# Performance work log

Measured on AMD Instinct MI355X. Metric: run time of the kernel, lower is better.

The kernel has to match this reference:

```python
import jax, jax.numpy as jnp
import numpy as np

LATENT, H, A, L, BOS = 256, 512, 64, 128, 0


def setup_inputs() -> dict:
    key = jax.random.key(0)
    ks = jax.random.split(key, 20)
    s = 0.05
    return {
        "latent": jax.random.normal(ks[0], (4096, LATENT), jnp.float32),
        "target": jax.random.normal(ks[1], (4096, L, A), jnp.float32),
        # latent dense decoder: Linear(LATENT,H), Tanh, Linear(H,H), Tanh, Linear(H,H)
        "Wd1": jax.random.normal(ks[2], (H, LATENT), jnp.float32) * s,
        "bd1": jnp.zeros((H,), jnp.float32),
        "Wd2": jax.random.normal(ks[3], (H, H), jnp.float32) * s,
        "bd2": jnp.zeros((H,), jnp.float32),
        "Wd3": jax.random.normal(ks[4], (H, H), jnp.float32) * s,
        "bd3": jnp.zeros((H,), jnp.float32),
        # GRU (torch layout: W_ih [3H,A], W_hh [3H,H], gate order r,z,n)
        "W_ih": jax.random.normal(ks[5], (3 * H, A), jnp.float32) * s,
        "W_hh": jax.random.normal(ks[6], (3 * H, H), jnp.float32) * s,
        "b_ih": jnp.zeros((3 * H,), jnp.float32),
        "b_hh": jnp.zeros((3 * H,), jnp.float32),
        # per-step dense decoder: Linear(H,H), Tanh, Linear(H,A), Tanh, Linear(A,A)
        "Wm1": jax.random.normal(ks[7], (H, H), jnp.float32) * s,
        "bm1": jnp.zeros((H,), jnp.float32),
        "Wm2": jax.random.normal(ks[8], (A, H), jnp.float32) * s,
        "bm2": jnp.zeros((A,), jnp.float32),
        "Wm3": jax.random.normal(ks[9], (A, A), jnp.float32) * s,
        "bm3": jnp.zeros((A,), jnp.float32),
    }


def reference(latent, target, Wd1, bd1, Wd2, bd2, Wd3, bd3,
              W_ih, W_hh, b_ih, b_hh, Wm1, bm1, Wm2, bm2, Wm3, bm3):
    B = latent.shape[0]
    # initial hidden from latent: Linear-Tanh-Linear-Tanh-Linear
    h = jnp.tanh(latent @ Wd1.T + bd1)
    h = jnp.tanh(h @ Wd2.T + bd2)
    h = h @ Wd3.T + bd3  # [B, H]

    # BOS pseudo one-hot: -16 everywhere, +16 at BOS index
    bos = jnp.full((B, A), -16.0, jnp.float32).at[:, BOS].set(16.0)

    # teacher forcing: step i (1..L-1) consumes [bos, target[:,1], ..., target[:,L-2]]
    xs = jnp.concatenate([bos[None], jnp.swapaxes(target[:, 1:L - 1], 0, 1)], axis=0)  # [L-1, B, A]

    def step(h, x):
        gi = x @ W_ih.T + b_ih  # [B, 3H]
        gh = h @ W_hh.T + b_hh
        ir, iz, inn = jnp.split(gi, 3, axis=-1)
        hr, hz, hn = jnp.split(gh, 3, axis=-1)
        r = jax.nn.sigmoid(ir + hr)
        z = jax.nn.sigmoid(iz + hz)
        n = jnp.tanh(inn + r * hn)
        h_new = (1.0 - z) * n + z * h
        p = jnp.tanh(h_new @ Wm1.T + bm1)
        p = jnp.tanh(p @ Wm2.T + bm2)
        pred = p @ Wm3.T + bm3  # [B, A]
        return h_new, pred

    _, preds = jax.lax.scan(step, h, xs)  # preds: [L-1, B, A]
    y = jnp.concatenate([bos[None], preds], axis=0)  # [L, B, A]
    return jnp.swapaxes(y, 0, 1)  # [B, L, A]
```

## Files before the change

### kernel.cpp

```cpp
#include <hip/hip_runtime.h>
#include <math.h>
#include <stdint.h>

#define BATCH 4096
#define LATENT 256
#define H 512
#define A 64
#define SEQL 128
#define KCAT 576
#define NSTEP 127
#define SEGLEN 16
#define NSEG 8

#define MB 256
#define JB 32
#define BST 584
#define AS_ELEMS (3 * 256 * 32)
#define BS_ELEMS (96 * BST)
#define GRU_LDS ((AS_ELEMS + BS_ELEMS) * 2)

typedef __bf16 bf16x8 __attribute__((ext_vector_type(8)));
typedef float f32x4 __attribute__((ext_vector_type(4)));
typedef uint16_t u16x8 __attribute__((ext_vector_type(8)));

__device__ __forceinline__ uint16_t f2bf(float f) {
    union { float f; uint32_t u; } v; v.f = f;
    uint32_t u = v.u + 0x7FFFu + ((v.u >> 16) & 1u);
    return (uint16_t)(u >> 16);
}

__device__ __forceinline__ float fast_sig(float x) {
    return __fdividef(1.0f, 1.0f + __expf(-x));
}
__device__ __forceinline__ float fast_tanh(float x) {
    return __fdividef(2.0f, 1.0f + __expf(-2.0f * x)) - 1.0f;
}

__device__ __forceinline__ f32x4 mfma16(bf16x8 a, bf16x8 b, f32x4 c) {
    return __builtin_amdgcn_mfma_f32_16x16x32_bf16(a, b, c, 0, 0, 0);
}

__device__ __forceinline__ void load_lds16(const void* g, void* l) {
    __builtin_amdgcn_global_load_lds(
        (const __attribute__((address_space(1))) uint32_t*)g,
        (__attribute__((address_space(3))) uint32_t*)l, 16, 0, 0);
}


__global__ __launch_bounds__(256) void cvt_bf16_kernel(const float* __restrict__ src,
                                                       uint16_t* __restrict__ dst, int n) {
    int idx = (blockIdx.x * 256 + threadIdx.x) * 4;
    if (idx < n) {
        float4 v = *(const float4*)(src + idx);
        dst[idx + 0] = f2bf(v.x); dst[idx + 1] = f2bf(v.y);
        dst[idx + 2] = f2bf(v.z); dst[idx + 3] = f2bf(v.w);
    }
}

__global__ __launch_bounds__(256) void wcat_kernel(const float* __restrict__ W_ih,
                                                   const float* __restrict__ W_hh,
                                                   uint16_t* __restrict__ Wcat) {
    int idx = blockIdx.x * 256 + threadIdx.x;
    if (idx < 1536 * KCAT) {
        int row = idx / KCAT, col = idx - row * KCAT;
        float v = (col < 64) ? W_ih[row * 64 + col] : W_hh[row * 512 + col - 64];
        Wcat[idx] = f2bf(v);
    }
}

__global__ __launch_bounds__(256) void bias_kernel(const float* __restrict__ b_ih,
                                                   const float* __restrict__ b_hh,
                                                   float* __restrict__ biases) {
    int idx = blockIdx.x * 256 + threadIdx.x;
    if (idx < 2048) {
        int seg = idx >> 9, j = idx & 511;
        float v;
        if (seg == 0) v = b_ih[j] + b_hh[j];
        else if (seg == 1) v = b_ih[512 + j] + b_hh[512 + j];
        else if (seg == 2) v = b_ih[1024 + j];
        else v = b_hh[1024 + j];
        biases[idx] = v;
    }
}

__global__ __launch_bounds__(256) void xseg_kernel(const float* __restrict__ target,
                                                   uint16_t* __restrict__ X,
                                                   int t0, int ns) {
    int idx = blockIdx.x * 256 + threadIdx.x;
    int e = idx * 4;
    int a = e & 63;
    int b = (e >> 6) & (BATCH - 1);
    int sl = e >> 18;
    int t = t0 + sl;
    ushort4 o;
    if (t == 0) {
        o.x = f2bf((a == 0) ? 16.0f : -16.0f);
        uint16_t m16 = f2bf(-16.0f);
        o.y = m16; o.z = m16; o.w = m16;
    } else {
        float4 v = *(const float4*)(target + ((size_t)b * SEQL + t) * A + a);
        o.x = f2bf(v.x); o.y = f2bf(v.y); o.z = f2bf(v.z); o.w = f2bf(v.w);
    }
    *(ushort4*)(X + e) = o;
}

__global__ __launch_bounds__(256) void bosout_kernel(float* __restrict__ out) {
    int idx = blockIdx.x * 256 + threadIdx.x;
    int a = idx & (A - 1);
    int b = idx >> 6;
    out[(size_t)b * SEQL * A + a] = (a == 0) ? 16.0f : -16.0f;
}

__global__ __launch_bounds__(256)
void gemm_kernel(const uint16_t* __restrict__ Abf, int lda,
                 const uint16_t* __restrict__ Wbf,
                 const float* __restrict__ bias,
                 uint16_t* __restrict__ outb, float* __restrict__ outf,
                 int ldc, int K, int do_tanh)
{
    __shared__ __align__(16) uint16_t As[128 * 32];
    __shared__ __align__(16) uint16_t Bs[128 * 32];

    const int tid = threadIdx.x;
    const int w = tid >> 6, l = tid & 63;
    const int quad = l >> 4, lan = l & 15;
    const int m0 = blockIdx.y * 128;
    const int n0 = blockIdx.x * 128;
    const int wm = (w >> 1) * 64;
    const int wn = (w & 1) * 64;

    f32x4 acc[4][4];
#pragma unroll
    for (int i = 0; i < 4; ++i)
#pragma unroll
        for (int j = 0; j < 4; ++j) acc[i][j] = (f32x4){0.f, 0.f, 0.f, 0.f};

    const int arow = (l >> 2);
    const int kc8 = (l & 3) * 8;

    for (int k0 = 0; k0 < K; k0 += 32) {
        __syncthreads();
#pragma unroll
        for (int i = 0; i < 2; ++i) {
            int row = i * 64 + w * 16 + arow;
            load_lds16(Abf + (size_t)(m0 + row) * lda + k0 + kc8,
                       As + i * 2048 + w * 512 + l * 8);
        }
#pragma unroll
        for (int i = 0; i < 2; ++i) {
            int row = i * 64 + w * 16 + arow;
            load_lds16(Wbf + (size_t)(n0 + row) * K + k0 + kc8,
                       Bs + i * 2048 + w * 512 + l * 8);
        }
        __syncthreads();

        bf16x8 af[4], bf[4];
#pragma unroll
        for (int mi = 0; mi < 4; ++mi)
            af[mi] = *(const bf16x8*)(As + (wm + mi * 16 + lan) * 32 + quad * 8);
#pragma unroll
        for (int nj = 0; nj < 4; ++nj)
            bf[nj] = *(const bf16x8*)(Bs + (wn + nj * 16 + lan) * 32 + quad * 8);
#pragma unroll
        for (int mi = 0; mi < 4; ++mi)
#pragma unroll
            for (int nj = 0; nj < 4; ++nj)
                acc[mi][nj] = mfma16(af[mi], bf[nj], acc[mi][nj]);
    }

#pragma unroll
    for (int mi = 0; mi < 4; ++mi) {
#pragma unroll
        for (int nj = 0; nj < 4; ++nj) {
#pragma unroll
            for (int reg = 0; reg < 4; ++reg) {
                int m = m0 + wm + mi * 16 + quad * 4 + reg;
                int n = n0 + wn + nj * 16 + lan;
                float v = acc[mi][nj][reg] + bias[n];
                if (do_tanh) v = fast_tanh(v);
                if (outf) outf[(size_t)m * ldc + n] = v;
                if (outb) outb[(size_t)m * ldc + n] = f2bf(v);
            }
        }
    }
}

__global__ __launch_bounds__(512)
void gru_seg_kernel(const uint16_t* __restrict__ Xseg,
                    const uint16_t* __restrict__ Wcat,
                    const float* __restrict__ biases,
                    const uint16_t* __restrict__ hprev0,
                    float* __restrict__ hA,
                    uint16_t* __restrict__ hall,
                    uint32_t* __restrict__ cnt,
                    int nsteps)
{
    extern __shared__ __align__(16) uint16_t lds[];
    uint16_t* As = lds;
    uint16_t* Bs = lds + AS_ELEMS;

    const int tid = threadIdx.x;
    const int bid = blockIdx.x;
    const int xcd = bid & 7;
    const int kk  = bid >> 3;
    const int jb  = kk & 15;
    const int mg  = xcd + ((kk >> 4) << 3);
    const int j0  = jb * JB;
    const int mbase = mg * MB;

    const int w = tid >> 6, l = tid & 63;
    const int quad = l >> 4, lan = l & 15;
    const int wm = (w >> 1) * 64;
    const int wj = (w & 1) * 16;
    const int jcol = j0 + wj + lan;

    float hreg[4][4];
#pragma unroll
    for (int mi = 0; mi < 4; ++mi)
#pragma unroll
        for (int r = 0; r < 4; ++r)
            hreg[mi][r] = hA[(size_t)(mbase + wm + mi * 16 + quad * 4 + r) * H + jcol];
    const float br = biases[jcol], bz = biases[512 + jcol];
    const float bi = biases[1024 + jcol], bh = biases[1536 + jcol];
    __builtin_amdgcn_sched_barrier(0);
    asm volatile("s_waitcnt vmcnt(0)");
    __builtin_amdgcn_sched_barrier(0);

    for (int i = tid; i < 96 * 72; i += 512) {
        int row = i / 72, c = i - row * 72;
        int wrow = ((row >> 5) << 9) + j0 + (row & 31);
        uint4 v = *(const uint4*)(Wcat + (size_t)wrow * KCAT + c * 8);
        *(uint4*)(Bs + row * BST + c * 8) = v;
    }
    __builtin_amdgcn_sched_barrier(0);

    auto stage = [&](int s2, int kt2, int bsel) {
        const uint16_t* P; int ld;
        if (kt2 < 2) { P = Xseg + ((size_t)s2 * BATCH + mbase) * 64 + kt2 * 32; ld = 64; }
        else {
            const uint16_t* hs = (s2 == 0) ? hprev0 : hall + (size_t)(s2 - 1) * (BATCH * H);
            P = hs + (size_t)mbase * H + (kt2 - 2) * 32; ld = 512;
        }
#pragma unroll
        for (int i = 0; i < 2; ++i) {
            int g = i * 512 + tid;
            int row = g & 255, c = g >> 8;
            load_lds16(P + (size_t)row * ld + c * 8, As + bsel * 8192 + g * 8);
        }
    };

    stage(0, 0, 0);
    stage(0, 1, 1);
    __builtin_amdgcn_sched_barrier(0);
    asm volatile("s_waitcnt lgkmcnt(0)");
    __builtin_amdgcn_s_barrier();
    __builtin_amdgcn_sched_barrier(0);

    f32x4 acc[4][4];
#pragma unroll
    for (int i = 0; i < 4; ++i)
#pragma unroll
        for (int j = 0; j < 4; ++j) acc[i][j] = (f32x4){0.f, 0.f, 0.f, 0.f};

    const int N = 18 * nsteps;
    int bufc = 0;

    for (int s = 0; s < nsteps; ++s) {
        for (int kt = 0; kt < 18; ++kt) {
            const int ts = s * 18 + kt;
            if (kt == 0 && s > 0) {
                if (tid == 0) {
                    const uint32_t* fl = cnt + mg * SEGLEN + (s - 1);
                    while (__hip_atomic_load(fl, __ATOMIC_RELAXED,
                                             __HIP_MEMORY_SCOPE_AGENT) < 16u)
                        __builtin_amdgcn_s_sleep(8);
                }
                __builtin_amdgcn_s_barrier();
                __builtin_amdgcn_sched_barrier(0);
            }
            if (ts + 2 < N) {
                int kt2 = kt + 2, s2 = s;
                if (kt2 >= 18) { kt2 -= 18; ++s2; }
                int sb = bufc + 2; if (sb >= 3) sb -= 3;
                stage(s2, kt2, sb);
            }
            __builtin_amdgcn_sched_barrier(0);
            if (ts + 2 < N)      asm volatile("s_waitcnt vmcnt(4)");
            else if (ts + 1 < N) asm volatile("s_waitcnt vmcnt(2)");
            else                 asm volatile("s_waitcnt vmcnt(0)");
            __builtin_amdgcn_sched_barrier(0);
            __builtin_amdgcn_s_barrier();
            __builtin_amdgcn_sched_barrier(0);

            bf16x8 af[4], bfr[3];
#pragma unroll
            for (int mi = 0; mi < 4; ++mi)
                af[mi] = *(const bf16x8*)(As + bufc * 8192 + quad * 2048 +
                                          (wm + mi * 16 + lan) * 8);
#pragma unroll
            for (int g = 0; g < 3; ++g)
                bfr[g] = *(const bf16x8*)(Bs + (g * 32 + wj + lan) * BST + kt * 32 + quad * 8);

#pragma unroll
            for (int mi = 0; mi < 4; ++mi) {
                acc[mi][0] = mfma16(af[mi], bfr[0], acc[mi][0]);
                acc[mi][1] = mfma16(af[mi], bfr[1], acc[mi][1]);
            }
            if (kt < 2) {
#pragma unroll
                for (int mi = 0; mi < 4; ++mi)
                    acc[mi][2] = mfma16(af[mi], bfr[2], acc[mi][2]);
            } else {
#pragma unroll
                for (int mi = 0; mi < 4; ++mi)
                    acc[mi][3] = mfma16(af[mi], bfr[2], acc[mi][3]);
            }
            __builtin_amdgcn_sched_barrier(0);
            __builtin_amdgcn_s_barrier();
            __builtin_amdgcn_sched_barrier(0);
            ++bufc; if (bufc >= 3) bufc = 0;
        }

        uint16_t* ht = hall + (size_t)s * (BATCH * H);
#pragma unroll
        for (int mi = 0; mi < 4; ++mi) {
#pragma unroll
            for (int r = 0; r < 4; ++r) {
                float R  = acc[mi][0][r] + br;
                float Z  = acc[mi][1][r] + bz;
                float I  = acc[mi][2][r] + bi;
                float HN = acc[mi][3][r] + bh;
                float rg = fast_sig(R);
                float zg = fast_sig(Z);
                float nn = fast_tanh(I + rg * HN);
                float hv = (1.0f - zg) * nn + zg * hreg[mi][r];
                hreg[mi][r] = hv;
                ht[(size_t)(mbase + wm + mi * 16 + quad * 4 + r) * H + jcol] = f2bf(hv);
                acc[mi][0][r] = 0.f; acc[mi][1][r] = 0.f;
                acc[mi][2][r] = 0.f; acc[mi][3][r] = 0.f;
            }
        }
        __syncthreads();
        if (tid == 0) {
            (void)__hip_atomic_fetch_add(cnt + mg * SEGLEN + s, 1u,
                                         __ATOMIC_RELEASE, __HIP_MEMORY_SCOPE_AGENT);
        }
    }

#pragma unroll
    for (int mi = 0; mi < 4; ++mi)
#pragma unroll
        for (int r = 0; r < 4; ++r)
            hA[(size_t)(mbase + wm + mi * 16 + quad * 4 + r) * H + jcol] = hreg[mi][r];
}

__global__ __launch_bounds__(256)
void d23_kernel(const uint16_t* __restrict__ p1,
                const uint16_t* __restrict__ Wm2,
                const float* __restrict__ bm2,
                const uint16_t* __restrict__ Wm3,
                const float* __restrict__ bm3,
                float* __restrict__ out, int t0)
{
    __shared__ __align__(16) uint16_t As[128 * 32];
    __shared__ __align__(16) uint16_t B2[64 * 32];
    __shared__ __align__(16) uint16_t W3[64 * 64];
    __shared__ __align__(16) uint16_t Ps[128 * 80];

    const int tid = threadIdx.x;
    const int w = tid >> 6, l = tid & 63;
    const int quad = l >> 4, lan = l & 15;
    const int m0 = blockIdx.y * 128;
    const int wm = w * 32;

#pragma unroll
    for (int i = 0; i < 2; ++i) {
        int g = i * 256 + tid;
        int row = g >> 3, kc = (g & 7) * 8;
        load_lds16(Wm3 + (size_t)row * 64 + kc, W3 + (size_t)g * 8);
    }

    f32x4 acc[2][4];
#pragma unroll
    for (int i = 0; i < 2; ++i)
#pragma unroll
        for (int j = 0; j < 4; ++j) acc[i][j] = (f32x4){0.f, 0.f, 0.f, 0.f};

    for (int k0 = 0; k0 < 512; k0 += 32) {
        __syncthreads();
#pragma unroll
        for (int i = 0; i < 2; ++i) {
            int g = i * 256 + tid;
            int row = g >> 2, kc = (g & 3) * 8;
            load_lds16(p1 + (size_t)(m0 + row) * 512 + k0 + kc, As + (size_t)g * 8);
        }
        {
            int g = tid;
            int row = g >> 2, kc = (g & 3) * 8;
            load_lds16(Wm2 + (size_t)row * 512 + k0 + kc, B2 + (size_t)g * 8);
        }
        __syncthreads();

        bf16x8 af[2], bf[4];
#pragma unroll
        for (int mi = 0; mi < 2; ++mi)
            af[mi] = *(const bf16x8*)(As + (wm + mi * 16 + lan) * 32 + quad * 8);
#pragma unroll
        for (int nj = 0; nj < 4; ++nj)
            bf[nj] = *(const bf16x8*)(B2 + (nj * 16 + lan) * 32 + quad * 8);
#pragma unroll
        for (int mi = 0; mi < 2; ++mi)
#pragma unroll
            for (int nj = 0; nj < 4; ++nj)
                acc[mi][nj] = mfma16(af[mi], bf[nj], acc[mi][nj]);
    }

#pragma unroll
    for (int mi = 0; mi < 2; ++mi)
#pragma unroll
        for (int nj = 0; nj < 4; ++nj)
#pragma unroll
            for (int reg = 0; reg < 4; ++reg) {
                int row = wm + mi * 16 + quad * 4 + reg;
                int n = nj * 16 + lan;
                float v = fast_tanh(acc[mi][nj][reg] + bm2[n]);
                Ps[row * 80 + n] = f2bf(v);
            }
    __syncthreads();

    f32x4 a3[2][4];
#pragma unroll
    for (int i = 0; i < 2; ++i)
#pragma unroll
        for (int j = 0; j < 4; ++j) a3[i][j] = (f32x4){0.f, 0.f, 0.f, 0.f};

#pragma unroll
    for (int ks = 0; ks < 64; ks += 32) {
        bf16x8 af[2], bf[4];
#pragma unroll
        for (int mi = 0; mi < 2; ++mi)
            af[mi] = *(const bf16x8*)(Ps + (wm + mi * 16 + lan) * 80 + ks + quad * 8);
#pragma unroll
        for (int nj = 0; nj < 4; ++nj)
            bf[nj] = *(const bf16x8*)(W3 + (nj * 16 + lan) * 64 + ks + quad * 8);
#pragma unroll
        for (int mi = 0; mi < 2; ++mi)
#pragma unroll
            for (int nj = 0; nj < 4; ++nj)
                a3[mi][nj] = mfma16(af[mi], bf[nj], a3[mi][nj]);
    }

#pragma unroll
    for (int mi = 0; mi < 2; ++mi)
#pragma unroll
        for (int nj = 0; nj < 4; ++nj)
#pragma unroll
            for (int reg = 0; reg < 4; ++reg) {
                int m = m0 + wm + mi * 16 + quad * 4 + reg;
                int n = nj * 16 + lan;
                int b = m & (BATCH - 1), tl = m >> 12;
                out[(size_t)b * SEQL * A + (size_t)(t0 + tl + 1) * A + n] =
                    a3[mi][nj][reg] + bm3[n];
            }
}


extern "C" void kernel_launch(void* const* d_in, const int* in_sizes, int n_in,
                              void* d_out, int out_size, void* d_ws, size_t ws_size,
                              hipStream_t stream)
{
    const float* latent = (const float*)d_in[0];
    const float* target = (const float*)d_in[1];
    const float* Wd1 = (const float*)d_in[2];
    const float* bd1 = (const float*)d_in[3];
    const float* Wd2 = (const float*)d_in[4];
    const float* bd2 = (const float*)d_in[5];
    const float* Wd3 = (const float*)d_in[6];
    const float* bd3 = (const float*)d_in[7];
    const float* W_ih = (const float*)d_in[8];
    const float* W_hh = (const float*)d_in[9];
    const float* b_ih = (const float*)d_in[10];
    const float* b_hh = (const float*)d_in[11];
    const float* Wm1 = (const float*)d_in[12];
    const float* bm1 = (const float*)d_in[13];
    const float* Wm2 = (const float*)d_in[14];
    const float* bm2 = (const float*)d_in[15];
    const float* Wm3 = (const float*)d_in[16];
    const float* bm3 = (const float*)d_in[17];

    float* out = (float*)d_out;
    uint8_t* ws = (uint8_t*)d_ws;

    size_t off = 0;
    auto carve = [&](size_t bytes) { void* p = ws + off; off += (bytes + 255) & ~(size_t)255; return p; };
    uint16_t* latb = (uint16_t*)carve((size_t)BATCH * LATENT * 2);
    uint16_t* wd1b = (uint16_t*)carve((size_t)H * LATENT * 2);
    uint16_t* wd2b = (uint16_t*)carve((size_t)H * H * 2);
    uint16_t* wd3b = (uint16_t*)carve((size_t)H * H * 2);
    uint16_t* wm1b = (uint16_t*)carve((size_t)H * H * 2);
    uint16_t* wm2b = (uint16_t*)carve((size_t)A * H * 2);
    uint16_t* wm3b = (uint16_t*)carve((size_t)A * A * 2);
    uint16_t* wcat = (uint16_t*)carve((size_t)1536 * KCAT * 2);
    float* biases  = (float*)carve(2048 * 4);
    uint16_t* t1b  = (uint16_t*)carve((size_t)BATCH * H * 2);
    uint16_t* t2b  = (uint16_t*)carve((size_t)BATCH * H * 2);
    uint16_t* h0bf = (uint16_t*)carve((size_t)BATCH * H * 2);
    float* hA      = (float*)carve((size_t)BATCH * H * 4);
    uint16_t* Xseg = (uint16_t*)carve((size_t)SEGLEN * BATCH * A * 2);
    uint16_t* hall = (uint16_t*)carve((size_t)SEGLEN * BATCH * H * 2);
    uint16_t* p1   = (uint16_t*)carve((size_t)8 * BATCH * H * 2);
    uint32_t* cnt  = (uint32_t*)carve((size_t)16 * SEGLEN * 4);

    static int attr_done = 0;
    if (!attr_done) {
        hipFuncSetAttribute((const void*)gru_seg_kernel,
                            hipFuncAttributeMaxDynamicSharedMemorySize, GRU_LDS);
        attr_done = 1;
    }

    dim3 blk(256);

    auto cvt = [&](const float* s, uint16_t* d, int n) {
        cvt_bf16_kernel<<<dim3((n / 4 + 255) / 256), blk, 0, stream>>>(s, d, n);
    };
    cvt(latent, latb, BATCH * LATENT);
    cvt(Wd1, wd1b, H * LATENT);
    cvt(Wd2, wd2b, H * H);
    cvt(Wd3, wd3b, H * H);
    cvt(Wm1, wm1b, H * H);
    cvt(Wm2, wm2b, A * H);
    cvt(Wm3, wm3b, A * A);
    wcat_kernel<<<dim3((1536 * KCAT + 255) / 256), blk, 0, stream>>>(W_ih, W_hh, wcat);
    bias_kernel<<<dim3(8), blk, 0, stream>>>(b_ih, b_hh, biases);
    bosout_kernel<<<dim3(BATCH * A / 256), blk, 0, stream>>>(out);

    gemm_kernel<<<dim3(H / 128, BATCH / 128), blk, 0, stream>>>(
        latb, LATENT, wd1b, bd1, t1b, nullptr, H, LATENT, 1);
    gemm_kernel<<<dim3(H / 128, BATCH / 128), blk, 0, stream>>>(
        t1b, H, wd2b, bd2, t2b, nullptr, H, H, 1);
    gemm_kernel<<<dim3(H / 128, BATCH / 128), blk, 0, stream>>>(
        t2b, H, wd3b, bd3, h0bf, hA, H, H, 0);

    for (int seg = 0; seg < NSEG; ++seg) {
        const int t0 = seg * SEGLEN;
        const int ns = (seg == NSEG - 1) ? (NSTEP - t0) : SEGLEN;
        xseg_kernel<<<dim3(ns * 256), blk, 0, stream>>>(target, Xseg, t0, ns);
        hipMemsetAsync(cnt, 0, (size_t)16 * SEGLEN * 4, stream);
        const uint16_t* hp0 = (seg == 0) ? h0bf : hall + (size_t)(SEGLEN - 1) * BATCH * H;
        gru_seg_kernel<<<dim3(256), dim3(512), GRU_LDS, stream>>>(
            Xseg, wcat, biases, hp0, hA, hall, cnt, ns);
        int done = 0;
        while (done < ns) {
            const int hw = (ns - done >= 8) ? 8 : (ns - done);
            const int M = hw * BATCH;
            gemm_kernel<<<dim3(H / 128, M / 128), blk, 0, stream>>>(
                hall + (size_t)done * BATCH * H, H, wm1b, bm1, p1, nullptr, H, H, 1);
            d23_kernel<<<dim3(1, M / 128), blk, 0, stream>>>(
                p1, wm2b, bm2, wm3b, bm3, out, t0 + done);
            done += hw;
        }
    }
}
```

Measured before the change: 3.723 ms.

## Store GRU hidden states and inputs in k-tiled 32-column layout

Changes the layout of the per-step hidden-state buffer, the initial hidden state and the input segment to a tiled [ktile][batch][32] format. The GRU kernel's A-tile staging then becomes one contiguous load per block instead of strided row loads, and LDS reads use a row-major 32-wide layout. The GEMM kernel gains flags to read tiled A and write tiled output. The GRU epilogue stores now write 64-byte rows per tile, which may change store coalescing, and the LDS read pattern changes bank behaviour.

```diff
diff --git a/kernel.cpp b/kernel.cpp
--- a/kernel.cpp
+++ b/kernel.cpp
@@ -21,7 +21,6 @@
 
 typedef __bf16 bf16x8 __attribute__((ext_vector_type(8)));
 typedef float f32x4 __attribute__((ext_vector_type(4)));
-typedef uint16_t u16x8 __attribute__((ext_vector_type(8)));
 
 __device__ __forceinline__ uint16_t f2bf(float f) {
     union { float f; uint32_t u; } v; v.f = f;
@@ -101,7 +100,8 @@
         float4 v = *(const float4*)(target + ((size_t)b * SEQL + t) * A + a);
         o.x = f2bf(v.x); o.y = f2bf(v.y); o.z = f2bf(v.z); o.w = f2bf(v.w);
     }
-    *(ushort4*)(X + e) = o;
+    size_t d = ((size_t)(sl * 2 + (a >> 5)) * BATCH + b) * 32 + (a & 31);
+    *(ushort4*)(X + d) = o;
 }
 
 __global__ __launch_bounds__(256) void bosout_kernel(float* __restrict__ out) {
@@ -116,7 +116,7 @@
                  const uint16_t* __restrict__ Wbf,
                  const float* __restrict__ bias,
                  uint16_t* __restrict__ outb, float* __restrict__ outf,
-                 int ldc, int K, int do_tanh)
+                 int ldc, int K, int do_tanh, int tiledA, int tiledOutB)
 {
     __shared__ __align__(16) uint16_t As[128 * 32];
     __shared__ __align__(16) uint16_t Bs[128 * 32];
@@ -143,8 +143,11 @@
 #pragma unroll
         for (int i = 0; i < 2; ++i) {
             int row = i * 64 + w * 16 + arow;
-            load_lds16(Abf + (size_t)(m0 + row) * lda + k0 + kc8,
-                       As + i * 2048 + w * 512 + l * 8);
+            int m = m0 + row;
+            const uint16_t* src = tiledA
+                ? Abf + ((size_t)((m >> 12) * 16 + (k0 >> 5)) * BATCH + (m & (BATCH - 1))) * 32 + kc8
+                : Abf + (size_t)m * lda + k0 + kc8;
+            load_lds16(src, As + i * 2048 + w * 512 + l * 8);
         }
 #pragma unroll
         for (int i = 0; i < 2; ++i) {
@@ -179,7 +182,12 @@
                 float v = acc[mi][nj][reg] + bias[n];
                 if (do_tanh) v = fast_tanh(v);
                 if (outf) outf[(size_t)m * ldc + n] = v;
-                if (outb) outb[(size_t)m * ldc + n] = f2bf(v);
+                if (outb) {
+                    size_t d = tiledOutB
+                        ? ((size_t)(n >> 5) * BATCH + m) * 32 + (n & 31)
+                        : (size_t)m * ldc + n;
+                    outb[d] = f2bf(v);
+                }
             }
         }
     }
@@ -189,9 +197,9 @@
 void gru_seg_kernel(const uint16_t* __restrict__ Xseg,
                     const uint16_t* __restrict__ Wcat,
                     const float* __restrict__ biases,
-                    const uint16_t* __restrict__ hprev0,
+                    const uint16_t* __restrict__ hprevT,
                     float* __restrict__ hA,
-                    uint16_t* __restrict__ hall,
+                    uint16_t* __restrict__ hall2,
                     uint32_t* __restrict__ cnt,
                     int nsteps)
 {
@@ -235,17 +243,14 @@
     __builtin_amdgcn_sched_barrier(0);
 
     auto stage = [&](int s2, int kt2, int bsel) {
-        const uint16_t* P; int ld;
-        if (kt2 < 2) { P = Xseg + ((size_t)s2 * BATCH + mbase) * 64 + kt2 * 32; ld = 64; }
-        else {
-            const uint16_t* hs = (s2 == 0) ? hprev0 : hall + (size_t)(s2 - 1) * (BATCH * H);
-            P = hs + (size_t)mbase * H + (kt2 - 2) * 32; ld = 512;
-        }
+        const uint16_t* tb;
+        if (kt2 < 2)       tb = Xseg   + ((size_t)(s2 * 2 + kt2) * BATCH + mbase) * 32;
+        else if (s2 == 0)  tb = hprevT + ((size_t)(kt2 - 2) * BATCH + mbase) * 32;
+        else               tb = hall2  + ((size_t)((s2 - 1) * 16 + (kt2 - 2)) * BATCH + mbase) * 32;
 #pragma unroll
         for (int i = 0; i < 2; ++i) {
             int g = i * 512 + tid;
-            int row = g & 255, c = g >> 8;
-            load_lds16(P + (size_t)row * ld + c * 8, As + bsel * 8192 + g * 8);
+            load_lds16(tb + (size_t)g * 8, As + bsel * 8192 + g * 8);
         }
     };
 
@@ -295,8 +300,8 @@
             bf16x8 af[4], bfr[3];
 #pragma unroll
             for (int mi = 0; mi < 4; ++mi)
-                af[mi] = *(const bf16x8*)(As + bufc * 8192 + quad * 2048 +
-                                          (wm + mi * 16 + lan) * 8);
+                af[mi] = *(const bf16x8*)(As + bufc * 8192 +
+                                          (wm + mi * 16 + lan) * 32 + quad * 8);
 #pragma unroll
             for (int g = 0; g < 3; ++g)
                 bfr[g] = *(const bf16x8*)(Bs + (g * 32 + wj + lan) * BST + kt * 32 + quad * 8);
@@ -321,7 +326,7 @@
             ++bufc; if (bufc >= 3) bufc = 0;
         }
 
-        uint16_t* ht = hall + (size_t)s * (BATCH * H);
+        uint16_t* ht = hall2 + ((size_t)(s * 16 + jb) * BATCH + mbase) * 32;
 #pragma unroll
         for (int mi = 0; mi < 4; ++mi) {
 #pragma unroll
@@ -335,7 +340,7 @@
                 float nn = fast_tanh(I + rg * HN);
                 float hv = (1.0f - zg) * nn + zg * hreg[mi][r];
                 hreg[mi][r] = hv;
-                ht[(size_t)(mbase + wm + mi * 16 + quad * 4 + r) * H + jcol] = f2bf(hv);
+                ht[(size_t)(wm + mi * 16 + quad * 4 + r) * 32 + wj + lan] = f2bf(hv);
                 acc[mi][0][r] = 0.f; acc[mi][1][r] = 0.f;
                 acc[mi][2][r] = 0.f; acc[mi][3][r] = 0.f;
             }
@@ -504,10 +509,10 @@
     float* biases  = (float*)carve(2048 * 4);
     uint16_t* t1b  = (uint16_t*)carve((size_t)BATCH * H * 2);
     uint16_t* t2b  = (uint16_t*)carve((size_t)BATCH * H * 2);
-    uint16_t* h0bf = (uint16_t*)carve((size_t)BATCH * H * 2);
+    uint16_t* h0t  = (uint16_t*)carve((size_t)BATCH * H * 2);
     float* hA      = (float*)carve((size_t)BATCH * H * 4);
     uint16_t* Xseg = (uint16_t*)carve((size_t)SEGLEN * BATCH * A * 2);
-    uint16_t* hall = (uint16_t*)carve((size_t)SEGLEN * BATCH * H * 2);
+    uint16_t* hall2= (uint16_t*)carve((size_t)SEGLEN * 16 * BATCH * 32 * 2);
     uint16_t* p1   = (uint16_t*)carve((size_t)8 * BATCH * H * 2);
     uint32_t* cnt  = (uint32_t*)carve((size_t)16 * SEGLEN * 4);
 
@@ -535,26 +540,28 @@
     bosout_kernel<<<dim3(BATCH * A / 256), blk, 0, stream>>>(out);
 
     gemm_kernel<<<dim3(H / 128, BATCH / 128), blk, 0, stream>>>(
-        latb, LATENT, wd1b, bd1, t1b, nullptr, H, LATENT, 1);
+        latb, LATENT, wd1b, bd1, t1b, nullptr, H, LATENT, 1, 0, 0);
     gemm_kernel<<<dim3(H / 128, BATCH / 128), blk, 0, stream>>>(
-        t1b, H, wd2b, bd2, t2b, nullptr, H, H, 1);
+        t1b, H, wd2b, bd2, t2b, nullptr, H, H, 1, 0, 0);
     gemm_kernel<<<dim3(H / 128, BATCH / 128), blk, 0, stream>>>(
-        t2b, H, wd3b, bd3, h0bf, hA, H, H, 0);
+        t2b, H, wd3b, bd3, h0t, hA, H, H, 0, 0, 1);
 
     for (int seg = 0; seg < NSEG; ++seg) {
         const int t0 = seg * SEGLEN;
         const int ns = (seg == NSEG - 1) ? (NSTEP - t0) : SEGLEN;
         xseg_kernel<<<dim3(ns * 256), blk, 0, stream>>>(target, Xseg, t0, ns);
         hipMemsetAsync(cnt, 0, (size_t)16 * SEGLEN * 4, stream);
-        const uint16_t* hp0 = (seg == 0) ? h0bf : hall + (size_t)(SEGLEN - 1) * BATCH * H;
+        const uint16_t* hp0 = (seg == 0)
+            ? h0t : hall2 + (size_t)(SEGLEN - 1) * 16 * BATCH * 32;
         gru_seg_kernel<<<dim3(256), dim3(512), GRU_LDS, stream>>>(
-            Xseg, wcat, biases, hp0, hA, hall, cnt, ns);
+            Xseg, wcat, biases, hp0, hA, hall2, cnt, ns);
         int done = 0;
         while (done < ns) {
             const int hw = (ns - done >= 8) ? 8 : (ns - done);
             const int M = hw * BATCH;
             gemm_kernel<<<dim3(H / 128, M / 128), blk, 0, stream>>>(
-                hall + (size_t)done * BATCH * H, H, wm1b, bm1, p1, nullptr, H, H, 1);
+                hall2 + (size_t)done * 16 * BATCH * 32, H, wm1b, bm1,
+                p1, nullptr, H, H, 1, 1, 0);
             d23_kernel<<<dim3(1, M / 128), blk, 0, stream>>>(
                 p1, wm2b, bm2, wm3b, bm3, out, t0 + done);
             done += hw;
```

New measurement: 3.861 ms. 1.04x slower.

## Store GRU inputs and hidden states in swizzled contiguous tiles shared across kernels

Applied to the files above, without the earlier changes.

The hidden-state history and the per-step inputs now live in one buffer laid out as contiguous 256x32 bf16 tiles with an XOR swizzle. The GRU kernel stages each tile with a single contiguous load into LDS and reads it without bank conflicts, and the Wm1 GEMM reads the same tiled layout directly. The last step's hidden state goes to a separate stash buffer so the next segment can start from it. The counter memset is hoisted out of the segment loop, the spin-wait sleep is shortened and an acquire fence is added, and the MFMA block runs at raised priority. The cost is more complex address arithmetic and an extra branch in the GEMM's A-loader.

```diff
diff --git a/kernel.cpp b/kernel.cpp
--- a/kernel.cpp
+++ b/kernel.cpp
@@ -19,9 +19,14 @@
 #define BS_ELEMS (96 * BST)
 #define GRU_LDS ((AS_ELEMS + BS_ELEMS) * 2)
 
+#define TILE_E 8192
+#define TS_E   (16 * TILE_E)
+#define STEP_E (18 * TS_E)
+#define HALL_E ((size_t)SEGLEN * STEP_E)
+#define STASH_E ((size_t)16 * 16 * TILE_E)
+
 typedef __bf16 bf16x8 __attribute__((ext_vector_type(8)));
 typedef float f32x4 __attribute__((ext_vector_type(4)));
-typedef uint16_t u16x8 __attribute__((ext_vector_type(8)));
 
 __device__ __forceinline__ uint16_t f2bf(float f) {
     union { float f; uint32_t u; } v; v.f = f;
@@ -44,6 +49,10 @@
     __builtin_amdgcn_global_load_lds(
         (const __attribute__((address_space(1))) uint32_t*)g,
         (__attribute__((address_space(3))) uint32_t*)l, 16, 0, 0);
+}
+
+__device__ __forceinline__ int cswz(int c, int row) {
+    return c ^ (row & 3) ^ ((row >> 2) & 3);
 }
 
 
@@ -84,7 +93,7 @@
 }
 
 __global__ __launch_bounds__(256) void xseg_kernel(const float* __restrict__ target,
-                                                   uint16_t* __restrict__ X,
+                                                   uint16_t* __restrict__ hall,
                                                    int t0, int ns) {
     int idx = blockIdx.x * 256 + threadIdx.x;
     int e = idx * 4;
@@ -101,7 +110,10 @@
         float4 v = *(const float4*)(target + ((size_t)b * SEQL + t) * A + a);
         o.x = f2bf(v.x); o.y = f2bf(v.y); o.z = f2bf(v.z); o.w = f2bf(v.w);
     }
-    *(ushort4*)(X + e) = o;
+    int rw = b & 255;
+    size_t d = (size_t)sl * STEP_E + (size_t)(a >> 5) * TS_E + (size_t)(b >> 8) * TILE_E
+             + (size_t)rw * 32 + cswz((a & 31) >> 3, rw) * 8 + (a & 7);
+    *(ushort4*)(hall + d) = o;
 }
 
 __global__ __launch_bounds__(256) void bosout_kernel(float* __restrict__ out) {
@@ -116,7 +128,9 @@
                  const uint16_t* __restrict__ Wbf,
                  const float* __restrict__ bias,
                  uint16_t* __restrict__ outb, float* __restrict__ outf,
-                 int ldc, int K, int do_tanh)
+                 int ldc, int K, int do_tanh, int tiledA, int tiledOutB,
+                 const uint16_t* __restrict__ hall, const uint16_t* __restrict__ stashA,
+                 int done, int stash_sl)
 {
     __shared__ __align__(16) uint16_t As[128 * 32];
     __shared__ __align__(16) uint16_t Bs[128 * 32];
@@ -140,11 +154,27 @@
 
     for (int k0 = 0; k0 < K; k0 += 32) {
         __syncthreads();
+        const uint16_t* abase = nullptr;
+        if (tiledA) {
+            int sstep = done + (m0 >> 12);
+            int kc = k0 >> 5;
+            int mg = (m0 >> 8) & 15;
+            abase = (sstep == stash_sl)
+                ? stashA + ((size_t)kc * 16 + mg) * TILE_E
+                : hall + (size_t)(sstep + 1) * STEP_E + (size_t)(2 + kc) * TS_E
+                       + (size_t)mg * TILE_E;
+        }
 #pragma unroll
         for (int i = 0; i < 2; ++i) {
             int row = i * 64 + w * 16 + arow;
-            load_lds16(Abf + (size_t)(m0 + row) * lda + k0 + kc8,
-                       As + i * 2048 + w * 512 + l * 8);
+            const uint16_t* src;
+            if (tiledA) {
+                int rowt = (m0 & 255) + row;
+                src = abase + (size_t)rowt * 32 + cswz(l & 3, rowt) * 8;
+            } else {
+                src = Abf + (size_t)(m0 + row) * lda + k0 + kc8;
+            }
+            load_lds16(src, As + i * 2048 + w * 512 + l * 8);
         }
 #pragma unroll
         for (int i = 0; i < 2; ++i) {
@@ -179,19 +209,28 @@
                 float v = acc[mi][nj][reg] + bias[n];
                 if (do_tanh) v = fast_tanh(v);
                 if (outf) outf[(size_t)m * ldc + n] = v;
-                if (outb) outb[(size_t)m * ldc + n] = f2bf(v);
+                if (outb) {
+                    size_t d;
+                    if (tiledOutB) {
+                        int rw = m & 255;
+                        d = ((size_t)(n >> 5) * 16 + (m >> 8)) * TILE_E
+                          + (size_t)rw * 32 + cswz((n & 31) >> 3, rw) * 8 + (n & 7);
+                    } else {
+                        d = (size_t)m * ldc + n;
+                    }
+                    outb[d] = f2bf(v);
+                }
             }
         }
     }
 }
 
 __global__ __launch_bounds__(512)
-void gru_seg_kernel(const uint16_t* __restrict__ Xseg,
+void gru_seg_kernel(uint16_t* hall,
+                    uint16_t* stash,
                     const uint16_t* __restrict__ Wcat,
                     const float* __restrict__ biases,
-                    const uint16_t* __restrict__ hprev0,
                     float* __restrict__ hA,
-                    uint16_t* __restrict__ hall,
                     uint32_t* __restrict__ cnt,
                     int nsteps)
 {
@@ -213,6 +252,7 @@
     const int wm = (w >> 1) * 64;
     const int wj = (w & 1) * 16;
     const int jcol = j0 + wj + lan;
+    const int xt = (lan & 3) ^ ((lan >> 2) & 3);
 
     float hreg[4][4];
 #pragma unroll
@@ -223,7 +263,7 @@
     const float br = biases[jcol], bz = biases[512 + jcol];
     const float bi = biases[1024 + jcol], bh = biases[1536 + jcol];
     __builtin_amdgcn_sched_barrier(0);
-    asm volatile("s_waitcnt vmcnt(0)");
+    asm volatile("s_waitcnt vmcnt(0)" ::: "memory");
     __builtin_amdgcn_sched_barrier(0);
 
     for (int i = tid; i < 96 * 72; i += 512) {
@@ -234,25 +274,17 @@
     }
     __builtin_amdgcn_sched_barrier(0);
 
-    auto stage = [&](int s2, int kt2, int bsel) {
-        const uint16_t* P; int ld;
-        if (kt2 < 2) { P = Xseg + ((size_t)s2 * BATCH + mbase) * 64 + kt2 * 32; ld = 64; }
-        else {
-            const uint16_t* hs = (s2 == 0) ? hprev0 : hall + (size_t)(s2 - 1) * (BATCH * H);
-            P = hs + (size_t)mbase * H + (kt2 - 2) * 32; ld = 512;
-        }
-#pragma unroll
-        for (int i = 0; i < 2; ++i) {
-            int g = i * 512 + tid;
-            int row = g & 255, c = g >> 8;
-            load_lds16(P + (size_t)row * ld + c * 8, As + bsel * 8192 + g * 8);
-        }
-    };
-
-    stage(0, 0, 0);
-    stage(0, 1, 1);
+    const size_t toff = (size_t)mg * TILE_E + (size_t)tid * 8;
+
+    {
+        const uint16_t* x0 = hall + toff;
+        load_lds16(x0,               As + tid * 8);
+        load_lds16(x0 + 4096,        As + 4096 + tid * 8);
+        load_lds16(x0 + TS_E,        As + TILE_E + tid * 8);
+        load_lds16(x0 + TS_E + 4096, As + TILE_E + 4096 + tid * 8);
+    }
     __builtin_amdgcn_sched_barrier(0);
-    asm volatile("s_waitcnt lgkmcnt(0)");
+    asm volatile("s_waitcnt lgkmcnt(0)" ::: "memory");
     __builtin_amdgcn_s_barrier();
     __builtin_amdgcn_sched_barrier(0);
 
@@ -262,66 +294,72 @@
 #pragma unroll
         for (int j = 0; j < 4; ++j) acc[i][j] = (f32x4){0.f, 0.f, 0.f, 0.f};
 
-    const int N = 18 * nsteps;
-    int bufc = 0;
-
     for (int s = 0; s < nsteps; ++s) {
+        const uint16_t* hb = (s == 0)
+            ? (stash + toff) - 2 * TS_E
+            : hall + (size_t)s * STEP_E + toff;
+        const int snx = (s + 1 < nsteps) ? (s + 1) : s;
+        const uint16_t* xn = hall + (size_t)snx * STEP_E + toff;
+
+#pragma unroll
         for (int kt = 0; kt < 18; ++kt) {
-            const int ts = s * 18 + kt;
             if (kt == 0 && s > 0) {
                 if (tid == 0) {
                     const uint32_t* fl = cnt + mg * SEGLEN + (s - 1);
                     while (__hip_atomic_load(fl, __ATOMIC_RELAXED,
                                              __HIP_MEMORY_SCOPE_AGENT) < 16u)
-                        __builtin_amdgcn_s_sleep(8);
+                        __builtin_amdgcn_s_sleep(2);
+                    __builtin_amdgcn_fence(__ATOMIC_ACQUIRE, "agent");
                 }
                 __builtin_amdgcn_s_barrier();
-                __builtin_amdgcn_sched_barrier(0);
-            }
-            if (ts + 2 < N) {
-                int kt2 = kt + 2, s2 = s;
-                if (kt2 >= 18) { kt2 -= 18; ++s2; }
-                int sb = bufc + 2; if (sb >= 3) sb -= 3;
-                stage(s2, kt2, sb);
-            }
+            }
+            {
+                const int sb = (kt + 2) % 3;
+                const uint16_t* src = (kt < 16) ? hb + (size_t)(kt + 2) * TS_E
+                                                : xn + (size_t)(kt - 16) * TS_E;
+                load_lds16(src,        As + sb * TILE_E + tid * 8);
+                load_lds16(src + 4096, As + sb * TILE_E + 4096 + tid * 8);
+            }
+            asm volatile("s_waitcnt vmcnt(4)" ::: "memory");
+            __builtin_amdgcn_s_barrier();
             __builtin_amdgcn_sched_barrier(0);
-            if (ts + 2 < N)      asm volatile("s_waitcnt vmcnt(4)");
-            else if (ts + 1 < N) asm volatile("s_waitcnt vmcnt(2)");
-            else                 asm volatile("s_waitcnt vmcnt(0)");
+
+            const uint16_t* Ab = As + (kt % 3) * TILE_E;
+            bf16x8 af[4], bfr[3];
+#pragma unroll
+            for (int mi = 0; mi < 4; ++mi) {
+                int row = wm + mi * 16 + lan;
+                af[mi] = *(const bf16x8*)(Ab + row * 32 + ((quad ^ xt) * 8));
+            }
+#pragma unroll
+            for (int g = 0; g < 3; ++g)
+                bfr[g] = *(const bf16x8*)(Bs + (g * 32 + wj + lan) * BST + kt * 32 + quad * 8);
+
+            __builtin_amdgcn_s_setprio(1);
+#pragma unroll
+            for (int mi = 0; mi < 4; ++mi) {
+                acc[mi][0] = mfma16(af[mi], bfr[0], acc[mi][0]);
+                acc[mi][1] = mfma16(af[mi], bfr[1], acc[mi][1]);
+            }
+            if (kt < 2) {
+#pragma unroll
+                for (int mi = 0; mi < 4; ++mi)
+                    acc[mi][2] = mfma16(af[mi], bfr[2], acc[mi][2]);
+            } else {
+#pragma unroll
+                for (int mi = 0; mi < 4; ++mi)
+                    acc[mi][3] = mfma16(af[mi], bfr[2], acc[mi][3]);
+            }
+            __builtin_amdgcn_s_setprio(0);
             __builtin_amdgcn_sched_barrier(0);
             __builtin_amdgcn_s_barrier();
             __builtin_amdgcn_sched_barrier(0);
-
-            bf16x8 af[4], bfr[3];
-#pragma unroll
-            for (int mi = 0; mi < 4; ++mi)
-                af[mi] = *(const bf16x8*)(As + bufc * 8192 + quad * 2048 +
-                                          (wm + mi * 16 + lan) * 8);
-#pragma unroll
-            for (int g = 0; g < 3; ++g)
-                bfr[g] = *(const bf16x8*)(Bs + (g * 32 + wj + lan) * BST + kt * 32 + quad * 8);
-
-#pragma unroll
-            for (int mi = 0; mi < 4; ++mi) {
-                acc[mi][0] = mfma16(af[mi], bfr[0], acc[mi][0]);
-                acc[mi][1] = mfma16(af[mi], bfr[1], acc[mi][1]);
-            }
-            if (kt < 2) {
-#pragma unroll
-                for (int mi = 0; mi < 4; ++mi)
-                    acc[mi][2] = mfma16(af[mi], bfr[2], acc[mi][2]);
-            } else {
-#pragma unroll
-                for (int mi = 0; mi < 4; ++mi)
-                    acc[mi][3] = mfma16(af[mi], bfr[2], acc[mi][3]);
-            }
-            __builtin_amdgcn_sched_barrier(0);
-            __builtin_amdgcn_s_barrier();
-            __builtin_amdgcn_sched_barrier(0);
-            ++bufc; if (bufc >= 3) bufc = 0;
-        }
-
-        uint16_t* ht = hall + (size_t)s * (BATCH * H);
+        }
+
+        uint16_t* wt = (s == 15)
+            ? stash + ((size_t)jb * 16 + mg) * TILE_E
+            : hall + (size_t)(s + 1) * STEP_E + (size_t)(2 + jb) * TS_E
+                   + (size_t)mg * TILE_E;
 #pragma unroll
         for (int mi = 0; mi < 4; ++mi) {
 #pragma unroll
@@ -335,7 +373,9 @@
                 float nn = fast_tanh(I + rg * HN);
                 float hv = (1.0f - zg) * nn + zg * hreg[mi][r];
                 hreg[mi][r] = hv;
-                ht[(size_t)(mbase + wm + mi * 16 + quad * 4 + r) * H + jcol] = f2bf(hv);
+                int row = wm + mi * 16 + quad * 4 + r;
+                int col = wj + lan;
+                wt[(size_t)row * 32 + cswz(col >> 3, row) * 8 + (col & 7)] = f2bf(hv);
                 acc[mi][0][r] = 0.f; acc[mi][1][r] = 0.f;
                 acc[mi][2][r] = 0.f; acc[mi][3][r] = 0.f;
             }
@@ -504,12 +544,11 @@
     float* biases  = (float*)carve(2048 * 4);
     uint16_t* t1b  = (uint16_t*)carve((size_t)BATCH * H * 2);
     uint16_t* t2b  = (uint16_t*)carve((size_t)BATCH * H * 2);
-    uint16_t* h0bf = (uint16_t*)carve((size_t)BATCH * H * 2);
     float* hA      = (float*)carve((size_t)BATCH * H * 4);
-    uint16_t* Xseg = (uint16_t*)carve((size_t)SEGLEN * BATCH * A * 2);
-    uint16_t* hall = (uint16_t*)carve((size_t)SEGLEN * BATCH * H * 2);
+    uint16_t* hall = (uint16_t*)carve(HALL_E * 2);
+    uint16_t* stash= (uint16_t*)carve(STASH_E * 2);
     uint16_t* p1   = (uint16_t*)carve((size_t)8 * BATCH * H * 2);
-    uint32_t* cnt  = (uint32_t*)carve((size_t)16 * SEGLEN * 4);
+    uint32_t* cnt  = (uint32_t*)carve((size_t)NSEG * 16 * SEGLEN * 4);
 
     static int attr_done = 0;
     if (!attr_done) {
@@ -533,28 +572,32 @@
     wcat_kernel<<<dim3((1536 * KCAT + 255) / 256), blk, 0, stream>>>(W_ih, W_hh, wcat);
     bias_kernel<<<dim3(8), blk, 0, stream>>>(b_ih, b_hh, biases);
     bosout_kernel<<<dim3(BATCH * A / 256), blk, 0, stream>>>(out);
+    hipMemsetAsync(cnt, 0, (size_t)NSEG * 16 * SEGLEN * 4, stream);
 
     gemm_kernel<<<dim3(H / 128, BATCH / 128), blk, 0, stream>>>(
-        latb, LATENT, wd1b, bd1, t1b, nullptr, H, LATENT, 1);
+        latb, LATENT, wd1b, bd1, t1b, nullptr, H, LATENT, 1, 0, 0,
+        nullptr, nullptr, 0, 0);
     gemm_kernel<<<dim3(H / 128, BATCH / 128), blk, 0, stream>>>(
-        t1b, H, wd2b, bd2, t2b, nullptr, H, H, 1);
+        t1b, H, wd2b, bd2, t2b, nullptr, H, H, 1, 0, 0,
+        nullptr, nullptr, 0, 0);
     gemm_kernel<<<dim3(H / 128, BATCH / 128), blk, 0, stream>>>(
-        t2b, H, wd3b, bd3, h0bf, hA, H, H, 0);
+        t2b, H, wd3b, bd3, stash, hA, H, H, 0, 0, 1,
+        nullptr, nullptr, 0, 0);
 
     for (int seg = 0; seg < NSEG; ++seg) {
         const int t0 = seg * SEGLEN;
         const int ns = (seg == NSEG - 1) ? (NSTEP - t0) : SEGLEN;
-        xseg_kernel<<<dim3(ns * 256), blk, 0, stream>>>(target, Xseg, t0, ns);
-        hipMemsetAsync(cnt, 0, (size_t)16 * SEGLEN * 4, stream);
-        const uint16_t* hp0 = (seg == 0) ? h0bf : hall + (size_t)(SEGLEN - 1) * BATCH * H;
+        const int stash_sl = (ns == 16) ? 15 : (1 << 30);
+        xseg_kernel<<<dim3(ns * 256), blk, 0, stream>>>(target, hall, t0, ns);
         gru_seg_kernel<<<dim3(256), dim3(512), GRU_LDS, stream>>>(
-            Xseg, wcat, biases, hp0, hA, hall, cnt, ns);
+            hall, stash, wcat, biases, hA, cnt + (size_t)seg * 16 * SEGLEN, ns);
         int done = 0;
         while (done < ns) {
             const int hw = (ns - done >= 8) ? 8 : (ns - done);
             const int M = hw * BATCH;
             gemm_kernel<<<dim3(H / 128, M / 128), blk, 0, stream>>>(
-                hall + (size_t)done * BATCH * H, H, wm1b, bm1, p1, nullptr, H, H, 1);
+                nullptr, 0, wm1b, bm1, p1, nullptr, H, H, 1, 1, 0,
+                hall, stash, done, stash_sl);
             d23_kernel<<<dim3(1, M / 128), blk, 0, stream>>>(
                 p1, wm2b, bm2, wm3b, bm3, out, t0 + done);
             done += hw;
```

Measured after the change: 3.355 ms. 9.9% less time.
